# Optimization experiments

Measured on AMD Instinct MI355X. Metric: run time of the kernel, lower is better.

Reference implementation:

```python
import jax, jax.numpy as jnp
import numpy as np
from jax import lax

F_SIZE = 128
N_HEADS = 8
HEAD_D = F_SIZE // N_HEADS
LANE_F = 64
NUM_PREDS = 6


def _layernorm(x, g, b, eps=1e-5):
    m = x.mean(-1, keepdims=True)
    v = jnp.var(x, axis=-1, keepdims=True)
    return (x - m) * lax.rsqrt(v + eps) * g + b


def _lstm_cell(x, h, c, wih, whh, bih, bhh):
    # PyTorch LSTMCell: gates ordered i, f, g, o
    gates = x @ wih.T + bih + h @ whh.T + bhh
    i, f, g, o = jnp.split(gates, 4, axis=-1)
    c2 = jax.nn.sigmoid(f) * c + jax.nn.sigmoid(i) * jnp.tanh(g)
    h2 = jax.nn.sigmoid(o) * jnp.tanh(c2)
    return h2, c2


def _to_xy(dl, yaw):
    return jnp.concatenate([dl * jnp.cos(yaw), dl * jnp.sin(yaw)], axis=-1)


def _attention(tok_pos, h_ego, h, lane_tok, key_mask, wq, wk, wv, wo, pos_w, pos_b):
    # tokens = [ego, vehicles], keys/values = [tokens, lanes]
    B = h_ego.shape[0]
    tok = jnp.concatenate([h_ego, h], axis=1) + tok_pos @ pos_w + pos_b  # [B,N1,F]
    kv = jnp.concatenate([tok, lane_tok], axis=1)  # [B,N1+L,F]
    q = (tok @ wq).reshape(B, -1, N_HEADS, HEAD_D)
    k = (kv @ wk).reshape(B, -1, N_HEADS, HEAD_D)
    v = (kv @ wv).reshape(B, -1, N_HEADS, HEAD_D)
    s = jnp.einsum('bqhd,bkhd->bhqk', q, k) / jnp.asarray(np.sqrt(HEAD_D), jnp.float32)
    s = jnp.where(key_mask[:, None, None, :] > 0, s, -1e9)
    a = jax.nn.softmax(s, axis=-1)
    o = jnp.einsum('bhqk,bkhd->bqhd', a, v).reshape(B, -1, F_SIZE) @ wo
    tok = tok + o
    return tok[:, :1], tok[:, 1:]


def _forward(input, init_pos, lane_input, mask_input, lane_mask,
             conv_w, conv_b, pos_w, pos_b,
             lane_w1, lane_b1, lane_w2, lane_b2, lane_to_f,
             wq, wk, wv, wo, ln_ego_g, ln_ego_b, ln_g, ln_b,
             ego_wih, ego_whh, ego_bih, ego_bhh,
             veh_wih, veh_whh, veh_bih, veh_bhh,
             out_ego_w, out_ego_b, out_w, out_b, len_pred):
    T, B, N1, _ = input.shape
    V = N1 - 1
    Hh = T - 2  # valid conv over time with kernel 3

    # shared conv_input applied to ego+vehicles at once (same weights in original)
    x = jnp.transpose(input, (1, 3, 2, 0))  # [B,2,N1,T]
    feat = lax.conv_general_dilated(x, conv_w, (1, 1), 'VALID',
                                    dimension_numbers=('NCHW', 'OIHW', 'NCHW'))
    feat = feat + conv_b[None, :, None, None]
    feat = jnp.transpose(feat, (3, 0, 2, 1))  # [Hh,B,N1,F]
    h_ego_seq, h_seq = feat[:, :, :1], feat[:, :, 1:]

    # lane embedding: per-point MLP + mean pool
    lanes = jax.nn.relu(lane_input @ lane_w1 + lane_b1)
    lanes = jax.nn.relu(lanes @ lane_w2 + lane_b2).mean(axis=2)  # [B,L,LANE_F]
    lane_tok = lanes @ lane_to_f  # [B,L,F]
    key_mask = jnp.concatenate([mask_input, lane_mask], axis=1)  # [B,N1+L]

    pos0 = init_pos[0]
    pe0, pv0 = pos0[:, :1], pos0[:, 1:]

    def cell_step(hx_ego, cx_ego, hx, cx, he, hv, pe, pv):
        tok_pos = jnp.concatenate([pe, pv], axis=1)
        ae, av = _attention(tok_pos, he, hv, lane_tok, key_mask, wq, wk, wv, wo, pos_w, pos_b)
        ae = _layernorm(ae.reshape(B, F_SIZE), ln_ego_g, ln_ego_b)
        av = _layernorm(av.reshape(B * V, F_SIZE), ln_g, ln_b)
        hx_ego, cx_ego = _lstm_cell(ae, hx_ego, cx_ego, ego_wih, ego_whh, ego_bih, ego_bhh)
        hx, cx = _lstm_cell(av, hx, cx, veh_wih, veh_whh, veh_bih, veh_bhh)
        return hx_ego, cx_ego, hx, cx

    def hist_step(carry, xs):
        hx_ego, cx_ego, hx, cx, pe, pv = carry
        he, hv, xe, xv = xs
        pe = pe + _to_xy(xe[..., 0:1], xe[..., 1:2])
        pv = pv + _to_xy(xv[..., 0:1], xv[..., 1:2])
        hx_ego, cx_ego, hx, cx = cell_step(hx_ego, cx_ego, hx, cx, he, hv, pe, pv)
        return (hx_ego, cx_ego, hx, cx, pe, pv), None

    carry0 = (jnp.zeros((B, F_SIZE)), jnp.zeros((B, F_SIZE)),
              jnp.zeros((B * V, F_SIZE)), jnp.zeros((B * V, F_SIZE)), pe0, pv0)
    xs = (h_ego_seq, h_seq, input[:Hh, :, :1, :].transpose(0, 1, 2, 3), input[:Hh, :, 1:, :])
    carry, _ = lax.scan(hist_step, carry0, xs)
    hx_ego, cx_ego, hx, cx, pe, pv = carry

    pe = jnp.repeat(pe[:, :, None, :], NUM_PREDS, axis=2)  # [B,1,P,2]
    pv = jnp.repeat(pv[:, :, None, :], NUM_PREDS, axis=2)  # [B,V,P,2]

    def pred_step(carry, _):
        hx_ego, cx_ego, hx, cx, pe, pv = carry
        he = hx_ego.reshape(B, 1, F_SIZE)
        hv = hx.reshape(B, V, F_SIZE)
        hx_ego, cx_ego, hx, cx = cell_step(hx_ego, cx_ego, hx, cx, he, hv,
                                           pe.mean(axis=2), pv.mean(axis=2))
        oe = (hx_ego @ out_ego_w + out_ego_b).reshape(B, 1, NUM_PREDS, 6)
        ov = (hx @ out_w + out_b).reshape(B, V, NUM_PREDS, 6)
        pe = pe + _to_xy(oe[..., 0:1], oe[..., 1:2])
        pv = pv + _to_xy(ov[..., 0:1], ov[..., 1:2])
        y = jnp.concatenate([
            jnp.concatenate([pe, oe[..., 2:6]], axis=-1),
            jnp.concatenate([pv, ov[..., 2:6]], axis=-1)], axis=1)  # [B,N1,P,6]
        return (hx_ego, cx_ego, hx, cx, pe, pv), y

    carry = (hx_ego, cx_ego, hx, cx, pe, pv)
    _, ys = lax.scan(pred_step, carry, None, length=len_pred)
    return ys  # [len_pred,B,N1,NUM_PREDS,6]


def setup_inputs() -> dict:
    key = jax.random.key(0)
    ks = jax.random.split(key, 40)
    B, T, N1, L, PTS = 128, 22, 32, 64, 10
    F, LF, G4, P6 = F_SIZE, LANE_F, 4 * F_SIZE, NUM_PREDS * 6
    s = 0.05
    inp = {}
    inp['input'] = jax.random.normal(ks[0], (T, B, N1, 2), jnp.float32) * 0.1
    inp['init_pos'] = jax.random.normal(ks[1], (1, B, N1, 2), jnp.float32) * 10.0
    inp['lane_input'] = jax.random.normal(ks[2], (B, L, PTS, 2), jnp.float32)
    inp['mask_input'] = jnp.ones((B, N1), jnp.float32)
    inp['lane_mask'] = jnp.ones((B, L), jnp.float32)
    inp['conv_w'] = jax.random.normal(ks[3], (F, 2, 1, 3), jnp.float32) * s
    inp['conv_b'] = jnp.zeros((F,), jnp.float32)
    inp['pos_w'] = jax.random.normal(ks[4], (2, F), jnp.float32) * s
    inp['pos_b'] = jnp.zeros((F,), jnp.float32)
    inp['lane_w1'] = jax.random.normal(ks[5], (2, LF), jnp.float32) * s
    inp['lane_b1'] = jnp.zeros((LF,), jnp.float32)
    inp['lane_w2'] = jax.random.normal(ks[6], (LF, LF), jnp.float32) * s
    inp['lane_b2'] = jnp.zeros((LF,), jnp.float32)
    inp['lane_to_f'] = jax.random.normal(ks[7], (LF, F), jnp.float32) * s
    inp['wq'] = jax.random.normal(ks[8], (F, F), jnp.float32) * s
    inp['wk'] = jax.random.normal(ks[9], (F, F), jnp.float32) * s
    inp['wv'] = jax.random.normal(ks[10], (F, F), jnp.float32) * s
    inp['wo'] = jax.random.normal(ks[11], (F, F), jnp.float32) * s
    inp['ln_ego_g'] = jnp.ones((F,), jnp.float32)
    inp['ln_ego_b'] = jnp.zeros((F,), jnp.float32)
    inp['ln_g'] = jnp.ones((F,), jnp.float32)
    inp['ln_b'] = jnp.zeros((F,), jnp.float32)
    inp['ego_wih'] = jax.random.normal(ks[12], (G4, F), jnp.float32) * s
    inp['ego_whh'] = jax.random.normal(ks[13], (G4, F), jnp.float32) * s
    inp['ego_bih'] = jnp.zeros((G4,), jnp.float32)
    inp['ego_bhh'] = jnp.zeros((G4,), jnp.float32)
    inp['veh_wih'] = jax.random.normal(ks[14], (G4, F), jnp.float32) * s
    inp['veh_whh'] = jax.random.normal(ks[15], (G4, F), jnp.float32) * s
    inp['veh_bih'] = jnp.zeros((G4,), jnp.float32)
    inp['veh_bhh'] = jnp.zeros((G4,), jnp.float32)
    inp['out_ego_w'] = jax.random.normal(ks[16], (F, P6), jnp.float32) * s
    inp['out_ego_b'] = jnp.zeros((P6,), jnp.float32)
    inp['out_w'] = jax.random.normal(ks[17], (F, P6), jnp.float32) * s
    inp['out_b'] = jnp.zeros((P6,), jnp.float32)
    inp['len_pred'] = 30
    return inp


def reference(input, init_pos, lane_input, mask_input, lane_mask,
              conv_w, conv_b, pos_w, pos_b,
              lane_w1, lane_b1, lane_w2, lane_b2, lane_to_f,
              wq, wk, wv, wo, ln_ego_g, ln_ego_b, ln_g, ln_b,
              ego_wih, ego_whh, ego_bih, ego_bhh,
              veh_wih, veh_whh, veh_bih, veh_bhh,
              out_ego_w, out_ego_b, out_w, out_b, len_pred):
    return _forward(input, init_pos, lane_input, mask_input, lane_mask,
                    conv_w, conv_b, pos_w, pos_b,
                    lane_w1, lane_b1, lane_w2, lane_b2, lane_to_f,
                    wq, wk, wv, wo, ln_ego_g, ln_ego_b, ln_g, ln_b,
                    ego_wih, ego_whh, ego_bih, ego_bhh,
                    veh_wih, veh_whh, veh_bih, veh_bhh,
                    out_ego_w, out_ego_b, out_w, out_b, len_pred)
```

## Files before the change

### kernel.cpp

```cpp
#include <hip/hip_runtime.h>
#include <hip/hip_bf16.h>
#include <math.h>

constexpr int B   = 128;
constexpr int N1  = 32;
constexpr int HH  = 20;
constexpr int L   = 64;
constexpr int PTS = 10;
constexpr int F   = 128;
constexpr int LF  = 64;
constexpr int NH  = 8;
constexpr int HD  = 16;
constexpr int KVN = 96;
constexpr int G4  = 512;
constexpr int NP  = 6;
constexpr int P6  = 36;
constexpr int LEN = 30;

__device__ __forceinline__ float sigmoidf(float x) { return 1.f / (1.f + expf(-x)); }


__global__ void k_lane_tok(const float* __restrict__ lane_input,
                           const float* __restrict__ w1, const float* __restrict__ b1,
                           const float* __restrict__ w2, const float* __restrict__ b2,
                           const float* __restrict__ to_f,
                           float* __restrict__ kvbuf) {
    int bl = blockIdx.x; int b = bl / L, l = bl % L;
    int tid = threadIdx.x;
    __shared__ float h1[PTS][LF];
    __shared__ float m[LF];
    const float* xin = lane_input + ((size_t)(b * L + l) * PTS) * 2;
    float w10 = w1[tid], w11 = w1[LF + tid], bb1 = b1[tid];
    for (int p = 0; p < PTS; ++p) {
        float v = xin[p * 2] * w10 + xin[p * 2 + 1] * w11 + bb1;
        h1[p][tid] = fmaxf(v, 0.f);
    }
    __syncthreads();
    float acc = 0.f;
    for (int p = 0; p < PTS; ++p) {
        float s = b2[tid];
        for (int h = 0; h < LF; ++h) s += h1[p][h] * w2[h * LF + tid];
        acc += fmaxf(s, 0.f);
    }
    m[tid] = acc * (1.f / PTS);
    __syncthreads();
    float* outp = kvbuf + ((size_t)(b * KVN) + 32 + l) * F;
    for (int f = tid; f < F; f += LF) {
        float s = 0.f;
        for (int j = 0; j < LF; ++j) s += m[j] * to_f[j * F + f];
        outp[f] = s;
    }
}

__global__ void k_lane_kv(const float* __restrict__ kvbuf,
                          const float* __restrict__ wk, const float* __restrict__ wv,
                          float* __restrict__ kb, float* __restrict__ vb) {
    int g = blockIdx.x & 7, b = blockIdx.x >> 3;
    int n0 = 32 + g * 8;
    int tid = threadIdx.x;
    int j = tid & 127, rh = tid >> 7;
    __shared__ float tok[8][F];
    for (int i = tid; i < 8 * F; i += 256) {
        int r = i >> 7, c = i & 127;
        tok[r][c] = kvbuf[((size_t)b * KVN + n0 + r) * F + c];
    }
    __syncthreads();
    float ak[4] = {0, 0, 0, 0}, av[4] = {0, 0, 0, 0};
    int r0 = rh * 4;
    for (int k2 = 0; k2 < F; ++k2) {
        float wkv = wk[k2 * F + j], wvv = wv[k2 * F + j];
#pragma unroll
        for (int r = 0; r < 4; ++r) {
            float x = tok[r0 + r][k2];
            ak[r] += x * wkv; av[r] += x * wvv;
        }
    }
#pragma unroll
    for (int r = 0; r < 4; ++r) {
        int n = n0 + r0 + r;
        kb[((size_t)b * KVN + n) * F + j] = ak[r];
        vb[((size_t)b * KVN + n) * F + j] = av[r];
    }
}

__global__ void k_hist_pos(const float* __restrict__ input,
                           const float* __restrict__ init_pos,
                           float* __restrict__ hist_pos,
                           float* __restrict__ pred_pos) {
    int idx = blockIdx.x * blockDim.x + threadIdx.x;
    if (idx >= B * N1) return;
    float px = init_pos[idx * 2], py = init_pos[idx * 2 + 1];
    int b = idx / N1, n = idx % N1;
    for (int t = 0; t < HH; ++t) {
        const float* ip = input + ((size_t)(t * B + b) * N1 + n) * 2;
        float dl = ip[0], yaw = ip[1];
        px += dl * cosf(yaw);
        py += dl * sinf(yaw);
        float* hp = hist_pos + ((size_t)(t * B + b) * N1 + n) * 2;
        hp[0] = px; hp[1] = py;
    }
#pragma unroll
    for (int p = 0; p < NP; ++p) {
        pred_pos[((size_t)idx * NP + p) * 2 + 0] = px;
        pred_pos[((size_t)idx * NP + p) * 2 + 1] = py;
    }
}

__global__ void k_transpose_all(const float* __restrict__ w0, const float* __restrict__ w1,
                                const float* __restrict__ w2, const float* __restrict__ w3,
                                float* __restrict__ wt) {
    int i = blockIdx.x * blockDim.x + threadIdx.x;
    if (i >= 4 * G4 * F) return;
    int m = i / (G4 * F), rem = i % (G4 * F);
    int j = rem / F, k2 = rem % F;
    const float* src = (m == 0) ? w0 : (m == 1) ? w1 : (m == 2) ? w2 : w3;
    wt[(size_t)m * G4 * F + (size_t)k2 * G4 + j] = src[rem];
}


__global__ void k_tok_qkv(const float* __restrict__ input, const float* __restrict__ hist_pos,
                          const float* __restrict__ h, const float* __restrict__ pred_pos,
                          const float* __restrict__ conv_w, const float* __restrict__ conv_b,
                          const float* __restrict__ pos_w, const float* __restrict__ pos_b,
                          const float* __restrict__ wq, const float* __restrict__ wk,
                          const float* __restrict__ wv,
                          float* __restrict__ kvbuf, float* __restrict__ qb,
                          float* __restrict__ kb, float* __restrict__ vb,
                          int mode, int t) {
    int g = blockIdx.x & 3, b = blockIdx.x >> 2;
    int n0 = g * 8;
    int tid = threadIdx.x;
    int j = tid & 127, rh = tid >> 7;
    __shared__ float tok[8][F];
    for (int i = tid; i < 8 * F; i += 256) {
        int r = i >> 7, c = i & 127;
        int n = n0 + r;
        float acc;
        if (mode == 0) {
            acc = conv_b[c];
#pragma unroll
            for (int kt = 0; kt < 3; ++kt) {
                const float* ip = input + ((size_t)((t + kt) * B + b) * N1 + n) * 2;
                acc += ip[0] * conv_w[(c * 2 + 0) * 3 + kt] + ip[1] * conv_w[(c * 2 + 1) * 3 + kt];
            }
            const float* hp = hist_pos + ((size_t)(t * B + b) * N1 + n) * 2;
            acc += hp[0] * pos_w[c] + hp[1] * pos_w[F + c] + pos_b[c];
        } else {
            const float* pp = pred_pos + ((size_t)(b * N1 + n)) * NP * 2;
            float mx = 0.f, my = 0.f;
#pragma unroll
            for (int p = 0; p < NP; ++p) { mx += pp[p * 2]; my += pp[p * 2 + 1]; }
            mx *= (1.f / NP); my *= (1.f / NP);
            acc = h[((size_t)b * N1 + n) * F + c] + mx * pos_w[c] + my * pos_w[F + c] + pos_b[c];
        }
        tok[r][c] = acc;
        kvbuf[((size_t)b * KVN + n) * F + c] = acc;
    }
    __syncthreads();
    float aq[4] = {0, 0, 0, 0}, ak[4] = {0, 0, 0, 0}, av[4] = {0, 0, 0, 0};
    int r0 = rh * 4;
    for (int k2 = 0; k2 < F; k2 += 2) {
        float wq0 = wq[k2 * F + j], wk0 = wk[k2 * F + j], wv0 = wv[k2 * F + j];
        float wq1 = wq[(k2 + 1) * F + j], wk1 = wk[(k2 + 1) * F + j], wv1 = wv[(k2 + 1) * F + j];
#pragma unroll
        for (int r = 0; r < 4; ++r) {
            float x0 = tok[r0 + r][k2], x1 = tok[r0 + r][k2 + 1];
            aq[r] += x0 * wq0 + x1 * wq1;
            ak[r] += x0 * wk0 + x1 * wk1;
            av[r] += x0 * wv0 + x1 * wv1;
        }
    }
#pragma unroll
    for (int r = 0; r < 4; ++r) {
        int n = n0 + r0 + r;
        qb[((size_t)b * N1 + n) * F + j]  = aq[r];
        kb[((size_t)b * KVN + n) * F + j] = ak[r];
        vb[((size_t)b * KVN + n) * F + j] = av[r];
    }
}

__global__ void k_attn(const float* __restrict__ qb, const float* __restrict__ kb,
                       const float* __restrict__ vb,
                       const float* __restrict__ mask_in, const float* __restrict__ lane_mask,
                       float* __restrict__ ao) {
    int h = blockIdx.x & 7, b = blockIdx.x >> 3;
    int tid = threadIdx.x;
    __shared__ float qh[N1][HD];
    __shared__ float kh[KVN][HD + 1];
    __shared__ float vh[KVN][HD + 1];
    __shared__ float mk[KVN];
    __shared__ float sc[N1][KVN + 1];
    for (int i = tid; i < N1 * HD; i += 128) {
        int qr = i >> 4, d = i & 15;
        qh[qr][d] = qb[((size_t)b * N1 + qr) * F + h * HD + d];
    }
    for (int i = tid; i < KVN * HD; i += 128) {
        int kc = i >> 4, d = i & 15;
        kh[kc][d] = kb[((size_t)b * KVN + kc) * F + h * HD + d];
        vh[kc][d] = vb[((size_t)b * KVN + kc) * F + h * HD + d];
    }
    if (tid < KVN)
        mk[tid] = (tid < N1) ? mask_in[b * N1 + tid] : lane_mask[b * L + (tid - N1)];
    __syncthreads();
    for (int i = tid; i < N1 * KVN; i += 128) {
        int qr = i / KVN, kc = i % KVN;
        float acc = 0.f;
#pragma unroll
        for (int d = 0; d < HD; ++d) acc += qh[qr][d] * kh[kc][d];
        sc[qr][kc] = (mk[kc] > 0.f) ? acc * 0.25f : -1e9f;
    }
    __syncthreads();
    if (tid < N1) {
        float mx = -1e30f;
        for (int kc = 0; kc < KVN; ++kc) mx = fmaxf(mx, sc[tid][kc]);
        float sum = 0.f;
        for (int kc = 0; kc < KVN; ++kc) { float e = expf(sc[tid][kc] - mx); sc[tid][kc] = e; sum += e; }
        float inv = 1.f / sum;
        for (int kc = 0; kc < KVN; ++kc) sc[tid][kc] *= inv;
    }
    __syncthreads();
    for (int i = tid; i < N1 * HD; i += 128) {
        int qr = i >> 4, d = i & 15;
        float acc = 0.f;
        for (int kc = 0; kc < KVN; ++kc) acc += sc[qr][kc] * vh[kc][d];
        ao[((size_t)b * N1 + qr) * F + h * HD + d] = acc;
    }
}

__global__ void k_proj_ln(const float* __restrict__ ao, const float* __restrict__ kvbuf,
                          const float* __restrict__ wo,
                          const float* __restrict__ ln_ego_g, const float* __restrict__ ln_ego_b,
                          const float* __restrict__ ln_g, const float* __restrict__ ln_b,
                          float* __restrict__ xln) {
    int gq = blockIdx.x & 3, b = blockIdx.x >> 2;
    int n0 = gq * 8;
    int tid = threadIdx.x;
    int j = tid & 127, rh = tid >> 7;
    __shared__ float arow[8][F];
    __shared__ float xb[8][F + 1];
    __shared__ float st[8][2];
    for (int i = tid; i < 8 * F; i += 256) {
        int r = i >> 7, c = i & 127;
        arow[r][c] = ao[((size_t)b * N1 + n0 + r) * F + c];
    }
    __syncthreads();
    float acc[4] = {0, 0, 0, 0};
    int r0 = rh * 4;
    for (int k2 = 0; k2 < F; k2 += 2) {
        float w0 = wo[k2 * F + j], w1 = wo[(k2 + 1) * F + j];
#pragma unroll
        for (int r = 0; r < 4; ++r)
            acc[r] += arow[r0 + r][k2] * w0 + arow[r0 + r][k2 + 1] * w1;
    }
#pragma unroll
    for (int r = 0; r < 4; ++r)
        xb[r0 + r][j] = kvbuf[((size_t)b * KVN + n0 + r0 + r) * F + j] + acc[r];
    __syncthreads();
    if (tid < 8) {
        float s1 = 0.f, s2 = 0.f;
        for (int c = 0; c < F; ++c) { float x = xb[tid][c]; s1 += x; s2 += x * x; }
        float mean = s1 * (1.f / F);
        float var = s2 * (1.f / F) - mean * mean;
        st[tid][0] = mean; st[tid][1] = rsqrtf(var + 1e-5f);
    }
    __syncthreads();
    for (int i = tid; i < 8 * F; i += 256) {
        int r = i >> 7, c = i & 127;
        int n = n0 + r;
        const float* g  = (n == 0) ? ln_ego_g : ln_g;
        const float* bb = (n == 0) ? ln_ego_b : ln_b;
        xln[((size_t)b * N1 + n) * F + c] = (xb[r][c] - st[r][0]) * st[r][1] * g[c] + bb[c];
    }
}

__global__ void k_lstm_pred(const float* __restrict__ xln,
                            const float* __restrict__ ego_wih_t, const float* __restrict__ ego_whh_t,
                            const float* __restrict__ ego_bih, const float* __restrict__ ego_bhh,
                            const float* __restrict__ veh_wih_t, const float* __restrict__ veh_whh_t,
                            const float* __restrict__ veh_bih, const float* __restrict__ veh_bhh,
                            float* __restrict__ h, float* __restrict__ c,
                            const float* __restrict__ out_ego_w, const float* __restrict__ out_ego_b,
                            const float* __restrict__ out_w, const float* __restrict__ out_b,
                            float* __restrict__ pred_pos, float* __restrict__ out,
                            int mode, int step) {
    int n = blockIdx.x >> 3, bg = blockIdx.x & 7;
    int b0 = bg * 16;
    int j = threadIdx.x;
    const float *wih, *whh, *bih, *bhh;
    if (n == 0) { wih = ego_wih_t; whh = ego_whh_t; bih = ego_bih; bhh = ego_bhh; }
    else        { wih = veh_wih_t; whh = veh_whh_t; bih = veh_bih; bhh = veh_bhh; }
    __shared__ float xr[16][F];
    __shared__ float hr2[16][F];
    __shared__ float gs[16][G4];
    for (int i = j; i < 16 * F; i += 512) {
        int r = i >> 7, k2 = i & 127;
        size_t bn = (size_t)(b0 + r) * N1 + n;
        xr[r][k2]  = xln[bn * F + k2];
        hr2[r][k2] = h[bn * F + k2];
    }
    __syncthreads();
    float acc[16];
    float bsum = bih[j] + bhh[j];
#pragma unroll
    for (int r = 0; r < 16; ++r) acc[r] = bsum;
    for (int k2 = 0; k2 < F; k2 += 4) {
        float wa0 = wih[(size_t)(k2    ) * G4 + j], wb0 = whh[(size_t)(k2    ) * G4 + j];
        float wa1 = wih[(size_t)(k2 + 1) * G4 + j], wb1 = whh[(size_t)(k2 + 1) * G4 + j];
        float wa2 = wih[(size_t)(k2 + 2) * G4 + j], wb2 = whh[(size_t)(k2 + 2) * G4 + j];
        float wa3 = wih[(size_t)(k2 + 3) * G4 + j], wb3 = whh[(size_t)(k2 + 3) * G4 + j];
#pragma unroll
        for (int r = 0; r < 16; ++r) {
            float x0 = xr[r][k2], x1 = xr[r][k2 + 1], x2 = xr[r][k2 + 2], x3 = xr[r][k2 + 3];
            float h0 = hr2[r][k2], h1 = hr2[r][k2 + 1], h2v = hr2[r][k2 + 2], h3 = hr2[r][k2 + 3];
            acc[r] += x0 * wa0 + x1 * wa1 + x2 * wa2 + x3 * wa3
                    + h0 * wb0 + h1 * wb1 + h2v * wb2 + h3 * wb3;
        }
    }
#pragma unroll
    for (int r = 0; r < 16; ++r) gs[r][j] = acc[r];
    __syncthreads();
    for (int i = j; i < 16 * F; i += 512) {
        int r = i >> 7, f = i & 127;
        size_t bn = (size_t)(b0 + r) * N1 + n;
        float ig = gs[r][f], fg = gs[r][F + f], gg = gs[r][2 * F + f], og = gs[r][3 * F + f];
        float cold = c[bn * F + f];
        float c2 = sigmoidf(fg) * cold + sigmoidf(ig) * tanhf(gg);
        float h2 = sigmoidf(og) * tanhf(c2);
        c[bn * F + f] = c2;
        h[bn * F + f] = h2;
        xr[r][f] = h2;
    }
    if (mode == 1) {
        const float* W  = (n == 0) ? out_ego_w : out_w;
        const float* bb = (n == 0) ? out_ego_b : out_b;
        __syncthreads();
        for (int i = j; i < 16 * P6; i += 512) {
            int r = i / P6, jj = i % P6;
            float a = bb[jj];
            for (int k2 = 0; k2 < F; ++k2) a += xr[r][k2] * W[k2 * P6 + jj];
            gs[r][jj] = a;
        }
        __syncthreads();
        if (j < 16 * NP) {
            int r = j / NP, p = j % NP;
            size_t bn = (size_t)(b0 + r) * N1 + n;
            float dl = gs[r][p * 6 + 0], yaw = gs[r][p * 6 + 1];
            float* pp = pred_pos + (bn * NP + p) * 2;
            float px = pp[0] + dl * cosf(yaw);
            float py = pp[1] + dl * sinf(yaw);
            pp[0] = px; pp[1] = py;
            float* y = out + (size_t)step * B * N1 * P6 + (bn * NP + p) * 6;
            y[0] = px; y[1] = py;
            y[2] = gs[r][p * 6 + 2]; y[3] = gs[r][p * 6 + 3];
            y[4] = gs[r][p * 6 + 4]; y[5] = gs[r][p * 6 + 5];
        }
    }
}

extern "C" void kernel_launch(void* const* d_in, const int* in_sizes, int n_in,
                              void* d_out, int out_size, void* d_ws, size_t ws_size,
                              hipStream_t stream) {
    const float* input      = (const float*)d_in[0];
    const float* init_pos   = (const float*)d_in[1];
    const float* lane_input = (const float*)d_in[2];
    const float* mask_input = (const float*)d_in[3];
    const float* lane_mask  = (const float*)d_in[4];
    const float* conv_w     = (const float*)d_in[5];
    const float* conv_b     = (const float*)d_in[6];
    const float* pos_w      = (const float*)d_in[7];
    const float* pos_b      = (const float*)d_in[8];
    const float* lane_w1    = (const float*)d_in[9];
    const float* lane_b1    = (const float*)d_in[10];
    const float* lane_w2    = (const float*)d_in[11];
    const float* lane_b2    = (const float*)d_in[12];
    const float* lane_to_f  = (const float*)d_in[13];
    const float* wq         = (const float*)d_in[14];
    const float* wk         = (const float*)d_in[15];
    const float* wv         = (const float*)d_in[16];
    const float* wo         = (const float*)d_in[17];
    const float* ln_ego_g   = (const float*)d_in[18];
    const float* ln_ego_b   = (const float*)d_in[19];
    const float* ln_g       = (const float*)d_in[20];
    const float* ln_b       = (const float*)d_in[21];
    const float* ego_wih    = (const float*)d_in[22];
    const float* ego_whh    = (const float*)d_in[23];
    const float* ego_bih    = (const float*)d_in[24];
    const float* ego_bhh    = (const float*)d_in[25];
    const float* veh_wih    = (const float*)d_in[26];
    const float* veh_whh    = (const float*)d_in[27];
    const float* veh_bih    = (const float*)d_in[28];
    const float* veh_bhh    = (const float*)d_in[29];
    const float* out_ego_w  = (const float*)d_in[30];
    const float* out_ego_b  = (const float*)d_in[31];
    const float* out_w      = (const float*)d_in[32];
    const float* out_b      = (const float*)d_in[33];

    float* out = (float*)d_out;
    float* ws = (float*)d_ws;

    float* kv       = ws;
    float* qb       = kv + (size_t)B * KVN * F;
    float* kb       = qb + (size_t)B * N1 * F;
    float* vb       = kb + (size_t)B * KVN * F;
    float* ao       = vb + (size_t)B * KVN * F;
    float* xln      = ao + (size_t)B * N1 * F;
    float* hbuf     = xln + (size_t)B * N1 * F;
    float* cbuf     = hbuf + (size_t)B * N1 * F;
    float* hist_pos = cbuf + (size_t)B * N1 * F;
    float* pred_pos = hist_pos + (size_t)HH * B * N1 * 2;
    float* wt       = pred_pos + (size_t)B * N1 * NP * 2;
    float* ego_wih_t = wt;
    float* ego_whh_t = wt + (size_t)G4 * F;
    float* veh_wih_t = wt + (size_t)2 * G4 * F;
    float* veh_whh_t = wt + (size_t)3 * G4 * F;

    hipMemsetAsync(hbuf, 0, (size_t)B * N1 * F * sizeof(float), stream);
    hipMemsetAsync(cbuf, 0, (size_t)B * N1 * F * sizeof(float), stream);
    k_lane_tok<<<B * L, 64, 0, stream>>>(lane_input, lane_w1, lane_b1, lane_w2, lane_b2,
                                         lane_to_f, kv);
    k_hist_pos<<<(B * N1 + 255) / 256, 256, 0, stream>>>(input, init_pos, hist_pos, pred_pos);
    k_transpose_all<<<(4 * G4 * F + 255) / 256, 256, 0, stream>>>(ego_wih, ego_whh, veh_wih,
                                                                  veh_whh, wt);
    k_lane_kv<<<B * 8, 256, 0, stream>>>(kv, wk, wv, kb, vb);

    for (int t = 0; t < HH; ++t) {
        k_tok_qkv<<<B * 4, 256, 0, stream>>>(input, hist_pos, hbuf, pred_pos,
                                             conv_w, conv_b, pos_w, pos_b,
                                             wq, wk, wv, kv, qb, kb, vb, 0, t);
        k_attn<<<B * NH, 128, 0, stream>>>(qb, kb, vb, mask_input, lane_mask, ao);
        k_proj_ln<<<B * 4, 256, 0, stream>>>(ao, kv, wo, ln_ego_g, ln_ego_b, ln_g, ln_b, xln);
        k_lstm_pred<<<N1 * 8, 512, 0, stream>>>(xln, ego_wih_t, ego_whh_t, ego_bih, ego_bhh,
                                                veh_wih_t, veh_whh_t, veh_bih, veh_bhh,
                                                hbuf, cbuf, out_ego_w, out_ego_b, out_w, out_b,
                                                pred_pos, out, 0, 0);
    }

    for (int s = 0; s < LEN; ++s) {
        k_tok_qkv<<<B * 4, 256, 0, stream>>>(input, hist_pos, hbuf, pred_pos,
                                             conv_w, conv_b, pos_w, pos_b,
                                             wq, wk, wv, kv, qb, kb, vb, 1, 0);
        k_attn<<<B * NH, 128, 0, stream>>>(qb, kb, vb, mask_input, lane_mask, ao);
        k_proj_ln<<<B * 4, 256, 0, stream>>>(ao, kv, wo, ln_ego_g, ln_ego_b, ln_g, ln_b, xln);
        k_lstm_pred<<<N1 * 8, 512, 0, stream>>>(xln, ego_wih_t, ego_whh_t, ego_bih, ego_bhh,
                                                veh_wih_t, veh_whh_t, veh_bih, veh_bhh,
                                                hbuf, cbuf, out_ego_w, out_ego_b, out_w, out_b,
                                                pred_pos, out, 1, s);
    }
}
```

Baseline: 5.338 ms.

## Fuse the whole recurrent loop into one persistent per-batch megakernel

Replaces the 200 per-step launches (tok/qkv, attention, projection+layernorm, LSTM) with a single kernel of 128 blocks, one per batch element, that runs all 50 steps with tokens, Q/K/V, scores and hidden state held in shared memory. LSTM weights are repacked into an interleaved 8-wide layout, and wq/wk/wv/wo into float4 tuples, so each load is vectorised. The aim is to remove launch overhead and global round-trips between stages. The cost is that only 128 blocks occupy the GPU, leaving many CUs idle and making each step serial within a block.

```diff
diff --git a/kernel.cpp b/kernel.cpp
--- a/kernel.cpp
+++ b/kernel.cpp
@@ -106,254 +106,312 @@
     }
 }
 
-__global__ void k_transpose_all(const float* __restrict__ w0, const float* __restrict__ w1,
-                                const float* __restrict__ w2, const float* __restrict__ w3,
-                                float* __restrict__ wt) {
+__global__ void k_build_w8(const float* __restrict__ wih, const float* __restrict__ whh,
+                           float* __restrict__ w8) {
     int i = blockIdx.x * blockDim.x + threadIdx.x;
-    if (i >= 4 * G4 * F) return;
-    int m = i / (G4 * F), rem = i % (G4 * F);
-    int j = rem / F, k2 = rem % F;
-    const float* src = (m == 0) ? w0 : (m == 1) ? w1 : (m == 2) ? w2 : w3;
-    wt[(size_t)m * G4 * F + (size_t)k2 * G4 + j] = src[rem];
-}
-
-
-__global__ void k_tok_qkv(const float* __restrict__ input, const float* __restrict__ hist_pos,
-                          const float* __restrict__ h, const float* __restrict__ pred_pos,
-                          const float* __restrict__ conv_w, const float* __restrict__ conv_b,
-                          const float* __restrict__ pos_w, const float* __restrict__ pos_b,
-                          const float* __restrict__ wq, const float* __restrict__ wk,
-                          const float* __restrict__ wv,
-                          float* __restrict__ kvbuf, float* __restrict__ qb,
-                          float* __restrict__ kb, float* __restrict__ vb,
-                          int mode, int t) {
-    int g = blockIdx.x & 3, b = blockIdx.x >> 2;
-    int n0 = g * 8;
-    int tid = threadIdx.x;
-    int j = tid & 127, rh = tid >> 7;
-    __shared__ float tok[8][F];
-    for (int i = tid; i < 8 * F; i += 256) {
+    if (i >= 128 * 128 * 8) return;
+    int s = i & 7, f = (i >> 3) & 127, k = i >> 10;
+    w8[i] = (s < 4) ? wih[((size_t)(s * 128 + f)) * 128 + k]
+                    : whh[((size_t)((s - 4) * 128 + f)) * 128 + k];
+}
+
+__global__ void k_build_wqkvo(const float* __restrict__ wq, const float* __restrict__ wk,
+                              const float* __restrict__ wv, const float* __restrict__ wo,
+                              float4* __restrict__ out4) {
+    int i = blockIdx.x * blockDim.x + threadIdx.x;
+    if (i >= 128 * 128) return;
+    out4[i] = make_float4(wq[i], wk[i], wv[i], wo[i]);
+}
+
+__global__ __launch_bounds__(1024) void k_mega(
+    const float* __restrict__ input, const float* __restrict__ hist_pos,
+    const float* __restrict__ conv_w, const float* __restrict__ conv_b,
+    const float* __restrict__ pos_w, const float* __restrict__ pos_b,
+    const float4* __restrict__ wqkvo,
+    const float* __restrict__ ln_ego_g, const float* __restrict__ ln_ego_b,
+    const float* __restrict__ ln_g, const float* __restrict__ ln_b,
+    const float* __restrict__ egoW8, const float* __restrict__ vehW8,
+    const float* __restrict__ ego_bih, const float* __restrict__ ego_bhh,
+    const float* __restrict__ veh_bih, const float* __restrict__ veh_bhh,
+    const float* __restrict__ out_ego_w, const float* __restrict__ out_ego_b,
+    const float* __restrict__ out_w, const float* __restrict__ out_b,
+    const float* __restrict__ mask_input, const float* __restrict__ lane_mask,
+    const float* __restrict__ lane_kb, const float* __restrict__ lane_vb,
+    float* __restrict__ pred_pos, float* __restrict__ cbuf,
+    float* __restrict__ out)
+{
+    const int b = blockIdx.x;
+    const int tid = threadIdx.x;
+
+    __shared__ float  Kbuf[96 * 129];
+    __shared__ float4 Vt4[128 * 25];
+    __shared__ float  tokS[32 * 128];
+    __shared__ float  qsS[32 * 128];
+    __shared__ float  hsS[32 * 128];
+    __shared__ float4 sc4[32 * 24];
+    __shared__ float  mkS[96];
+
+    float* VtF = (float*)Vt4;
+    float* scF = (float*)sc4;
+
+    const int f  = tid & 127;
+    const int ng = tid >> 7;
+    const int n0 = ng * 4;
+
+    float bv[4], be[4];
+#pragma unroll
+    for (int g = 0; g < 4; ++g) {
+        bv[g] = veh_bih[g * 128 + f] + veh_bhh[g * 128 + f];
+        be[g] = ego_bih[g * 128 + f] + ego_bhh[g * 128 + f];
+    }
+
+    for (int i = tid; i < 64 * 128; i += 1024) {
         int r = i >> 7, c = i & 127;
-        int n = n0 + r;
-        float acc;
-        if (mode == 0) {
-            acc = conv_b[c];
-#pragma unroll
-            for (int kt = 0; kt < 3; ++kt) {
-                const float* ip = input + ((size_t)((t + kt) * B + b) * N1 + n) * 2;
-                acc += ip[0] * conv_w[(c * 2 + 0) * 3 + kt] + ip[1] * conv_w[(c * 2 + 1) * 3 + kt];
-            }
-            const float* hp = hist_pos + ((size_t)(t * B + b) * N1 + n) * 2;
-            acc += hp[0] * pos_w[c] + hp[1] * pos_w[F + c] + pos_b[c];
-        } else {
-            const float* pp = pred_pos + ((size_t)(b * N1 + n)) * NP * 2;
-            float mx = 0.f, my = 0.f;
-#pragma unroll
-            for (int p = 0; p < NP; ++p) { mx += pp[p * 2]; my += pp[p * 2 + 1]; }
-            mx *= (1.f / NP); my *= (1.f / NP);
-            acc = h[((size_t)b * N1 + n) * F + c] + mx * pos_w[c] + my * pos_w[F + c] + pos_b[c];
-        }
-        tok[r][c] = acc;
-        kvbuf[((size_t)b * KVN + n) * F + c] = acc;
-    }
+        float kvv = lane_kb[((size_t)b * KVN + 32 + r) * F + c];
+        float vvv = lane_vb[((size_t)b * KVN + 32 + r) * F + c];
+        Kbuf[(32 + r) * 129 + c] = kvv;
+        VtF[c * 100 + 32 + r]    = vvv;
+    }
+    for (int i = tid; i < 32 * 128; i += 1024) hsS[i] = 0.f;
+    if (tid < 96) mkS[tid] = (tid < 32) ? mask_input[b * 32 + tid] : lane_mask[b * 64 + tid - 32];
     __syncthreads();
-    float aq[4] = {0, 0, 0, 0}, ak[4] = {0, 0, 0, 0}, av[4] = {0, 0, 0, 0};
-    int r0 = rh * 4;
-    for (int k2 = 0; k2 < F; k2 += 2) {
-        float wq0 = wq[k2 * F + j], wk0 = wk[k2 * F + j], wv0 = wv[k2 * F + j];
-        float wq1 = wq[(k2 + 1) * F + j], wk1 = wk[(k2 + 1) * F + j], wv1 = wv[(k2 + 1) * F + j];
-#pragma unroll
-        for (int r = 0; r < 4; ++r) {
-            float x0 = tok[r0 + r][k2], x1 = tok[r0 + r][k2 + 1];
-            aq[r] += x0 * wq0 + x1 * wq1;
-            ak[r] += x0 * wk0 + x1 * wk1;
-            av[r] += x0 * wv0 + x1 * wv1;
-        }
-    }
-#pragma unroll
-    for (int r = 0; r < 4; ++r) {
-        int n = n0 + r0 + r;
-        qb[((size_t)b * N1 + n) * F + j]  = aq[r];
-        kb[((size_t)b * KVN + n) * F + j] = ak[r];
-        vb[((size_t)b * KVN + n) * F + j] = av[r];
-    }
-}
-
-__global__ void k_attn(const float* __restrict__ qb, const float* __restrict__ kb,
-                       const float* __restrict__ vb,
-                       const float* __restrict__ mask_in, const float* __restrict__ lane_mask,
-                       float* __restrict__ ao) {
-    int h = blockIdx.x & 7, b = blockIdx.x >> 3;
-    int tid = threadIdx.x;
-    __shared__ float qh[N1][HD];
-    __shared__ float kh[KVN][HD + 1];
-    __shared__ float vh[KVN][HD + 1];
-    __shared__ float mk[KVN];
-    __shared__ float sc[N1][KVN + 1];
-    for (int i = tid; i < N1 * HD; i += 128) {
-        int qr = i >> 4, d = i & 15;
-        qh[qr][d] = qb[((size_t)b * N1 + qr) * F + h * HD + d];
-    }
-    for (int i = tid; i < KVN * HD; i += 128) {
-        int kc = i >> 4, d = i & 15;
-        kh[kc][d] = kb[((size_t)b * KVN + kc) * F + h * HD + d];
-        vh[kc][d] = vb[((size_t)b * KVN + kc) * F + h * HD + d];
-    }
-    if (tid < KVN)
-        mk[tid] = (tid < N1) ? mask_in[b * N1 + tid] : lane_mask[b * L + (tid - N1)];
-    __syncthreads();
-    for (int i = tid; i < N1 * KVN; i += 128) {
-        int qr = i / KVN, kc = i % KVN;
-        float acc = 0.f;
-#pragma unroll
-        for (int d = 0; d < HD; ++d) acc += qh[qr][d] * kh[kc][d];
-        sc[qr][kc] = (mk[kc] > 0.f) ? acc * 0.25f : -1e9f;
-    }
-    __syncthreads();
-    if (tid < N1) {
-        float mx = -1e30f;
-        for (int kc = 0; kc < KVN; ++kc) mx = fmaxf(mx, sc[tid][kc]);
-        float sum = 0.f;
-        for (int kc = 0; kc < KVN; ++kc) { float e = expf(sc[tid][kc] - mx); sc[tid][kc] = e; sum += e; }
-        float inv = 1.f / sum;
-        for (int kc = 0; kc < KVN; ++kc) sc[tid][kc] *= inv;
-    }
-    __syncthreads();
-    for (int i = tid; i < N1 * HD; i += 128) {
-        int qr = i >> 4, d = i & 15;
-        float acc = 0.f;
-        for (int kc = 0; kc < KVN; ++kc) acc += sc[qr][kc] * vh[kc][d];
-        ao[((size_t)b * N1 + qr) * F + h * HD + d] = acc;
-    }
-}
-
-__global__ void k_proj_ln(const float* __restrict__ ao, const float* __restrict__ kvbuf,
-                          const float* __restrict__ wo,
-                          const float* __restrict__ ln_ego_g, const float* __restrict__ ln_ego_b,
-                          const float* __restrict__ ln_g, const float* __restrict__ ln_b,
-                          float* __restrict__ xln) {
-    int gq = blockIdx.x & 3, b = blockIdx.x >> 2;
-    int n0 = gq * 8;
-    int tid = threadIdx.x;
-    int j = tid & 127, rh = tid >> 7;
-    __shared__ float arow[8][F];
-    __shared__ float xb[8][F + 1];
-    __shared__ float st[8][2];
-    for (int i = tid; i < 8 * F; i += 256) {
-        int r = i >> 7, c = i & 127;
-        arow[r][c] = ao[((size_t)b * N1 + n0 + r) * F + c];
-    }
-    __syncthreads();
-    float acc[4] = {0, 0, 0, 0};
-    int r0 = rh * 4;
-    for (int k2 = 0; k2 < F; k2 += 2) {
-        float w0 = wo[k2 * F + j], w1 = wo[(k2 + 1) * F + j];
-#pragma unroll
-        for (int r = 0; r < 4; ++r)
-            acc[r] += arow[r0 + r][k2] * w0 + arow[r0 + r][k2 + 1] * w1;
-    }
-#pragma unroll
-    for (int r = 0; r < 4; ++r)
-        xb[r0 + r][j] = kvbuf[((size_t)b * KVN + n0 + r0 + r) * F + j] + acc[r];
-    __syncthreads();
-    if (tid < 8) {
-        float s1 = 0.f, s2 = 0.f;
-        for (int c = 0; c < F; ++c) { float x = xb[tid][c]; s1 += x; s2 += x * x; }
-        float mean = s1 * (1.f / F);
-        float var = s2 * (1.f / F) - mean * mean;
-        st[tid][0] = mean; st[tid][1] = rsqrtf(var + 1e-5f);
-    }
-    __syncthreads();
-    for (int i = tid; i < 8 * F; i += 256) {
-        int r = i >> 7, c = i & 127;
-        int n = n0 + r;
-        const float* g  = (n == 0) ? ln_ego_g : ln_g;
-        const float* bb = (n == 0) ? ln_ego_b : ln_b;
-        xln[((size_t)b * N1 + n) * F + c] = (xb[r][c] - st[r][0]) * st[r][1] * g[c] + bb[c];
-    }
-}
-
-__global__ void k_lstm_pred(const float* __restrict__ xln,
-                            const float* __restrict__ ego_wih_t, const float* __restrict__ ego_whh_t,
-                            const float* __restrict__ ego_bih, const float* __restrict__ ego_bhh,
-                            const float* __restrict__ veh_wih_t, const float* __restrict__ veh_whh_t,
-                            const float* __restrict__ veh_bih, const float* __restrict__ veh_bhh,
-                            float* __restrict__ h, float* __restrict__ c,
-                            const float* __restrict__ out_ego_w, const float* __restrict__ out_ego_b,
-                            const float* __restrict__ out_w, const float* __restrict__ out_b,
-                            float* __restrict__ pred_pos, float* __restrict__ out,
-                            int mode, int step) {
-    int n = blockIdx.x >> 3, bg = blockIdx.x & 7;
-    int b0 = bg * 16;
-    int j = threadIdx.x;
-    const float *wih, *whh, *bih, *bhh;
-    if (n == 0) { wih = ego_wih_t; whh = ego_whh_t; bih = ego_bih; bhh = ego_bhh; }
-    else        { wih = veh_wih_t; whh = veh_whh_t; bih = veh_bih; bhh = veh_bhh; }
-    __shared__ float xr[16][F];
-    __shared__ float hr2[16][F];
-    __shared__ float gs[16][G4];
-    for (int i = j; i < 16 * F; i += 512) {
-        int r = i >> 7, k2 = i & 127;
-        size_t bn = (size_t)(b0 + r) * N1 + n;
-        xr[r][k2]  = xln[bn * F + k2];
-        hr2[r][k2] = h[bn * F + k2];
-    }
-    __syncthreads();
-    float acc[16];
-    float bsum = bih[j] + bhh[j];
-#pragma unroll
-    for (int r = 0; r < 16; ++r) acc[r] = bsum;
-    for (int k2 = 0; k2 < F; k2 += 4) {
-        float wa0 = wih[(size_t)(k2    ) * G4 + j], wb0 = whh[(size_t)(k2    ) * G4 + j];
-        float wa1 = wih[(size_t)(k2 + 1) * G4 + j], wb1 = whh[(size_t)(k2 + 1) * G4 + j];
-        float wa2 = wih[(size_t)(k2 + 2) * G4 + j], wb2 = whh[(size_t)(k2 + 2) * G4 + j];
-        float wa3 = wih[(size_t)(k2 + 3) * G4 + j], wb3 = whh[(size_t)(k2 + 3) * G4 + j];
-#pragma unroll
-        for (int r = 0; r < 16; ++r) {
-            float x0 = xr[r][k2], x1 = xr[r][k2 + 1], x2 = xr[r][k2 + 2], x3 = xr[r][k2 + 3];
-            float h0 = hr2[r][k2], h1 = hr2[r][k2 + 1], h2v = hr2[r][k2 + 2], h3 = hr2[r][k2 + 3];
-            acc[r] += x0 * wa0 + x1 * wa1 + x2 * wa2 + x3 * wa3
-                    + h0 * wb0 + h1 * wb1 + h2v * wb2 + h3 * wb3;
-        }
-    }
-#pragma unroll
-    for (int r = 0; r < 16; ++r) gs[r][j] = acc[r];
-    __syncthreads();
-    for (int i = j; i < 16 * F; i += 512) {
-        int r = i >> 7, f = i & 127;
-        size_t bn = (size_t)(b0 + r) * N1 + n;
-        float ig = gs[r][f], fg = gs[r][F + f], gg = gs[r][2 * F + f], og = gs[r][3 * F + f];
-        float cold = c[bn * F + f];
-        float c2 = sigmoidf(fg) * cold + sigmoidf(ig) * tanhf(gg);
-        float h2 = sigmoidf(og) * tanhf(c2);
-        c[bn * F + f] = c2;
-        h[bn * F + f] = h2;
-        xr[r][f] = h2;
-    }
-    if (mode == 1) {
-        const float* W  = (n == 0) ? out_ego_w : out_w;
-        const float* bb = (n == 0) ? out_ego_b : out_b;
+
+#pragma unroll 1
+    for (int step = 0; step < HH + LEN; ++step) {
+        const int mode = (step >= HH) ? 1 : 0;
+        const int t = mode ? 0 : step;
+
+        for (int i = tid; i < 32 * 128; i += 1024) {
+            int n = i >> 7, c = i & 127;
+            float acc;
+            if (mode == 0) {
+                acc = conv_b[c];
+#pragma unroll
+                for (int kt = 0; kt < 3; ++kt) {
+                    const float* ip = input + ((size_t)((t + kt) * B + b) * N1 + n) * 2;
+                    acc += ip[0] * conv_w[(c * 2 + 0) * 3 + kt] + ip[1] * conv_w[(c * 2 + 1) * 3 + kt];
+                }
+                const float* hp = hist_pos + ((size_t)(t * B + b) * N1 + n) * 2;
+                acc += hp[0] * pos_w[c] + hp[1] * pos_w[128 + c] + pos_b[c];
+            } else {
+                const float* pp = pred_pos + (size_t)b * 384 + n * 12;
+                float mx = 0.f, my = 0.f;
+#pragma unroll
+                for (int p = 0; p < 6; ++p) { mx += pp[p * 2]; my += pp[p * 2 + 1]; }
+                mx *= (1.f / 6.f); my *= (1.f / 6.f);
+                acc = hsS[i] + mx * pos_w[c] + my * pos_w[128 + c] + pos_b[c];
+            }
+            tokS[i] = acc;
+        }
         __syncthreads();
-        for (int i = j; i < 16 * P6; i += 512) {
-            int r = i / P6, jj = i % P6;
-            float a = bb[jj];
-            for (int k2 = 0; k2 < F; ++k2) a += xr[r][k2] * W[k2 * P6 + jj];
-            gs[r][jj] = a;
+
+        {
+            float aq[4] = {0, 0, 0, 0}, ak[4] = {0, 0, 0, 0}, av[4] = {0, 0, 0, 0};
+            for (int k2 = 0; k2 < 128; k2 += 4) {
+                float4 xv[4];
+#pragma unroll
+                for (int r = 0; r < 4; ++r) xv[r] = *(const float4*)&tokS[(n0 + r) * 128 + k2];
+#pragma unroll
+                for (int kk = 0; kk < 4; ++kk) {
+                    float4 w4 = wqkvo[(size_t)(k2 + kk) * 128 + f];
+#pragma unroll
+                    for (int r = 0; r < 4; ++r) {
+                        float x = (&xv[r].x)[kk];
+                        aq[r] += x * w4.x; ak[r] += x * w4.y; av[r] += x * w4.z;
+                    }
+                }
+            }
+#pragma unroll
+            for (int r = 0; r < 4; ++r) {
+                qsS[(n0 + r) * 128 + f]  = aq[r];
+                Kbuf[(n0 + r) * 129 + f] = ak[r];
+                VtF[f * 100 + n0 + r]    = av[r];
+            }
         }
         __syncthreads();
-        if (j < 16 * NP) {
-            int r = j / NP, p = j % NP;
-            size_t bn = (size_t)(b0 + r) * N1 + n;
-            float dl = gs[r][p * 6 + 0], yaw = gs[r][p * 6 + 1];
-            float* pp = pred_pos + (bn * NP + p) * 2;
-            float px = pp[0] + dl * cosf(yaw);
-            float py = pp[1] + dl * sinf(yaw);
-            pp[0] = px; pp[1] = py;
-            float* y = out + (size_t)step * B * N1 * P6 + (bn * NP + p) * 6;
-            y[0] = px; y[1] = py;
-            y[2] = gs[r][p * 6 + 2]; y[3] = gs[r][p * 6 + 3];
-            y[4] = gs[r][p * 6 + 4]; y[5] = gs[r][p * 6 + 5];
-        }
+
+#pragma unroll 1
+        for (int h = 0; h < NH; ++h) {
+            const int hb = h * 16;
+            if (tid < 512) {
+                const int lane = tid & 63;
+                const int rb = (tid >> 6) * 4;
+                const int k2ok = lane < 32;
+                float s0[4] = {0, 0, 0, 0}, s1[4] = {0, 0, 0, 0};
+                for (int d4 = 0; d4 < 16; d4 += 4) {
+                    float4 qv[4];
+#pragma unroll
+                    for (int r = 0; r < 4; ++r) qv[r] = *(const float4*)&qsS[(rb + r) * 128 + hb + d4];
+#pragma unroll
+                    for (int kk = 0; kk < 4; ++kk) {
+                        float kA = Kbuf[lane * 129 + hb + d4 + kk];
+                        float kB = k2ok ? Kbuf[(64 + lane) * 129 + hb + d4 + kk] : 0.f;
+#pragma unroll
+                        for (int r = 0; r < 4; ++r) {
+                            float q = (&qv[r].x)[kk];
+                            s0[r] += q * kA; s1[r] += q * kB;
+                        }
+                    }
+                }
+                float mA = mkS[lane];
+                float mB = k2ok ? mkS[64 + lane] : 0.f;
+#pragma unroll
+                for (int r = 0; r < 4; ++r) {
+                    float v0 = (mA > 0.f) ? s0[r] * 0.25f : -1e9f;
+                    float v1 = (k2ok && mB > 0.f) ? s1[r] * 0.25f : -1e9f;
+                    float m = fmaxf(v0, v1);
+#pragma unroll
+                    for (int off = 32; off; off >>= 1) m = fmaxf(m, __shfl_xor(m, off));
+                    float e0 = expf(v0 - m);
+                    float e1 = k2ok ? expf(v1 - m) : 0.f;
+                    float s = e0 + e1;
+#pragma unroll
+                    for (int off = 32; off; off >>= 1) s += __shfl_xor(s, off);
+                    float inv = 1.f / s;
+                    scF[(rb + r) * 96 + lane] = e0 * inv;
+                    if (k2ok) scF[(rb + r) * 96 + 64 + lane] = e1 * inv;
+                }
+            }
+            __syncthreads();
+            if (tid < 512) {
+                const int qr = tid >> 4, d = tid & 15;
+                const float4* vrow = Vt4 + (hb + d) * 25;
+                const float4* srow = sc4 + qr * 24;
+                float acc = 0.f;
+#pragma unroll
+                for (int q4 = 0; q4 < 24; ++q4) {
+                    float4 pf = srow[q4], vv = vrow[q4];
+                    acc += pf.x * vv.x + pf.y * vv.y + pf.z * vv.z + pf.w * vv.w;
+                }
+                qsS[qr * 128 + hb + d] = acc;
+            }
+            __syncthreads();
+        }
+
+        {
+            float ac[4] = {0, 0, 0, 0};
+            for (int k2 = 0; k2 < 128; k2 += 4) {
+                float4 av4[4];
+#pragma unroll
+                for (int r = 0; r < 4; ++r) av4[r] = *(const float4*)&qsS[(n0 + r) * 128 + k2];
+#pragma unroll
+                for (int kk = 0; kk < 4; ++kk) {
+                    float4 w4 = wqkvo[(size_t)(k2 + kk) * 128 + f];
+#pragma unroll
+                    for (int r = 0; r < 4; ++r) ac[r] += (&av4[r].x)[kk] * w4.w;
+                }
+            }
+#pragma unroll
+            for (int r = 0; r < 4; ++r) tokS[(n0 + r) * 128 + f] += ac[r];
+        }
+        __syncthreads();
+
+        {
+            const int row = tid >> 5, l = tid & 31;
+            float x0 = tokS[row * 128 + l],      x1 = tokS[row * 128 + l + 32];
+            float x2 = tokS[row * 128 + l + 64], x3 = tokS[row * 128 + l + 96];
+            float s1v = x0 + x1 + x2 + x3;
+            float s2v = x0 * x0 + x1 * x1 + x2 * x2 + x3 * x3;
+#pragma unroll
+            for (int off = 16; off; off >>= 1) {
+                s1v += __shfl_xor(s1v, off, 32);
+                s2v += __shfl_xor(s2v, off, 32);
+            }
+            float mean = s1v * (1.f / 128.f);
+            float rs = rsqrtf(s2v * (1.f / 128.f) - mean * mean + 1e-5f);
+            const float* gg = (row == 0) ? ln_ego_g : ln_g;
+            const float* bb = (row == 0) ? ln_ego_b : ln_b;
+            tokS[row * 128 + l]      = (x0 - mean) * rs * gg[l]      + bb[l];
+            tokS[row * 128 + l + 32] = (x1 - mean) * rs * gg[l + 32] + bb[l + 32];
+            tokS[row * 128 + l + 64] = (x2 - mean) * rs * gg[l + 64] + bb[l + 64];
+            tokS[row * 128 + l + 96] = (x3 - mean) * rs * gg[l + 96] + bb[l + 96];
+        }
+        __syncthreads();
+
+        {
+            float acc[4][4];
+#pragma unroll
+            for (int r = 0; r < 4; ++r)
+#pragma unroll
+                for (int g = 0; g < 4; ++g) acc[r][g] = bv[g];
+            for (int k2 = 0; k2 < 128; k2 += 4) {
+                float4 xv[4], hv[4];
+#pragma unroll
+                for (int r = 0; r < 4; ++r) {
+                    xv[r] = *(const float4*)&tokS[(n0 + r) * 128 + k2];
+                    hv[r] = *(const float4*)&hsS[(n0 + r) * 128 + k2];
+                }
+#pragma unroll
+                for (int kk = 0; kk < 4; ++kk) {
+                    const float4* wp = (const float4*)&vehW8[((size_t)(k2 + kk) * 128 + f) * 8];
+                    float4 wi = wp[0], wh = wp[1];
+#pragma unroll
+                    for (int r = 0; r < 4; ++r) {
+                        float x = (&xv[r].x)[kk], hc = (&hv[r].x)[kk];
+                        acc[r][0] += x * wi.x + hc * wh.x;
+                        acc[r][1] += x * wi.y + hc * wh.y;
+                        acc[r][2] += x * wi.z + hc * wh.z;
+                        acc[r][3] += x * wi.w + hc * wh.w;
+                    }
+                }
+            }
+            if (ng == 0) {
+                float ae[4] = {be[0], be[1], be[2], be[3]};
+                for (int k2 = 0; k2 < 128; k2 += 4) {
+                    float4 xv = *(const float4*)&tokS[k2];
+                    float4 hv = *(const float4*)&hsS[k2];
+#pragma unroll
+                    for (int kk = 0; kk < 4; ++kk) {
+                        const float4* wp = (const float4*)&egoW8[((size_t)(k2 + kk) * 128 + f) * 8];
+                        float4 wi = wp[0], wh = wp[1];
+                        float x = (&xv.x)[kk], hc = (&hv.x)[kk];
+                        ae[0] += x * wi.x + hc * wh.x;
+                        ae[1] += x * wi.y + hc * wh.y;
+                        ae[2] += x * wi.z + hc * wh.z;
+                        ae[3] += x * wi.w + hc * wh.w;
+                    }
+                }
+#pragma unroll
+                for (int g = 0; g < 4; ++g) acc[0][g] = ae[g];
+            }
+            __syncthreads();
+#pragma unroll
+            for (int r = 0; r < 4; ++r) {
+                int n = n0 + r;
+                size_t cix = ((size_t)b * 32 + n) * 128 + f;
+                float c2 = sigmoidf(acc[r][1]) * cbuf[cix] + sigmoidf(acc[r][0]) * tanhf(acc[r][2]);
+                float h2 = sigmoidf(acc[r][3]) * tanhf(c2);
+                cbuf[cix] = c2;
+                hsS[n * 128 + f] = h2;
+            }
+        }
+
+        if (mode) {
+            __syncthreads();
+            for (int i = tid; i < 32 * 36; i += 1024) {
+                int n = i / 36, jj = i - n * 36;
+                const float* W = (n == 0) ? out_ego_w : out_w;
+                float a = (n == 0) ? out_ego_b[jj] : out_b[jj];
+                const float* hr = &hsS[n * 128];
+#pragma unroll 4
+                for (int k2 = 0; k2 < 128; ++k2) a += hr[k2] * W[k2 * 36 + jj];
+                scF[i] = a;
+            }
+            __syncthreads();
+            if (tid < 192) {
+                int n = tid / 6, p = tid - n * 6;
+                float dl = scF[n * 36 + p * 6], yaw = scF[n * 36 + p * 6 + 1];
+                float* pp = pred_pos + (size_t)b * 384 + n * 12 + p * 2;
+                float px = pp[0] + dl * cosf(yaw);
+                float py = pp[1] + dl * sinf(yaw);
+                pp[0] = px; pp[1] = py;
+                float* y = out + (size_t)(step - HH) * (B * N1 * P6) + ((size_t)b * 32 + n) * 36 + p * 6;
+                y[0] = px; y[1] = py;
+                y[2] = scF[n * 36 + p * 6 + 2]; y[3] = scF[n * 36 + p * 6 + 3];
+                y[4] = scF[n * 36 + p * 6 + 4]; y[5] = scF[n * 36 + p * 6 + 5];
+            }
+        }
+        __syncthreads();
     }
 }
 
@@ -399,51 +457,28 @@
     float* ws = (float*)d_ws;
 
     float* kv       = ws;
-    float* qb       = kv + (size_t)B * KVN * F;
-    float* kb       = qb + (size_t)B * N1 * F;
+    float* kb       = kv + (size_t)B * KVN * F;
     float* vb       = kb + (size_t)B * KVN * F;
-    float* ao       = vb + (size_t)B * KVN * F;
-    float* xln      = ao + (size_t)B * N1 * F;
-    float* hbuf     = xln + (size_t)B * N1 * F;
-    float* cbuf     = hbuf + (size_t)B * N1 * F;
+    float* cbuf     = vb + (size_t)B * KVN * F;
     float* hist_pos = cbuf + (size_t)B * N1 * F;
     float* pred_pos = hist_pos + (size_t)HH * B * N1 * 2;
-    float* wt       = pred_pos + (size_t)B * N1 * NP * 2;
-    float* ego_wih_t = wt;
-    float* ego_whh_t = wt + (size_t)G4 * F;
-    float* veh_wih_t = wt + (size_t)2 * G4 * F;
-    float* veh_whh_t = wt + (size_t)3 * G4 * F;
-
-    hipMemsetAsync(hbuf, 0, (size_t)B * N1 * F * sizeof(float), stream);
+    float* egoW8    = pred_pos + (size_t)B * N1 * NP * 2;
+    float* vehW8    = egoW8 + (size_t)128 * 128 * 8;
+    float* wqkvo    = vehW8 + (size_t)128 * 128 * 8;
+
     hipMemsetAsync(cbuf, 0, (size_t)B * N1 * F * sizeof(float), stream);
     k_lane_tok<<<B * L, 64, 0, stream>>>(lane_input, lane_w1, lane_b1, lane_w2, lane_b2,
                                          lane_to_f, kv);
     k_hist_pos<<<(B * N1 + 255) / 256, 256, 0, stream>>>(input, init_pos, hist_pos, pred_pos);
-    k_transpose_all<<<(4 * G4 * F + 255) / 256, 256, 0, stream>>>(ego_wih, ego_whh, veh_wih,
-                                                                  veh_whh, wt);
+    k_build_w8<<<(128 * 128 * 8 + 255) / 256, 256, 0, stream>>>(ego_wih, ego_whh, egoW8);
+    k_build_w8<<<(128 * 128 * 8 + 255) / 256, 256, 0, stream>>>(veh_wih, veh_whh, vehW8);
+    k_build_wqkvo<<<(128 * 128 + 255) / 256, 256, 0, stream>>>(wq, wk, wv, wo, (float4*)wqkvo);
     k_lane_kv<<<B * 8, 256, 0, stream>>>(kv, wk, wv, kb, vb);
 
-    for (int t = 0; t < HH; ++t) {
-        k_tok_qkv<<<B * 4, 256, 0, stream>>>(input, hist_pos, hbuf, pred_pos,
-                                             conv_w, conv_b, pos_w, pos_b,
-                                             wq, wk, wv, kv, qb, kb, vb, 0, t);
-        k_attn<<<B * NH, 128, 0, stream>>>(qb, kb, vb, mask_input, lane_mask, ao);
-        k_proj_ln<<<B * 4, 256, 0, stream>>>(ao, kv, wo, ln_ego_g, ln_ego_b, ln_g, ln_b, xln);
-        k_lstm_pred<<<N1 * 8, 512, 0, stream>>>(xln, ego_wih_t, ego_whh_t, ego_bih, ego_bhh,
-                                                veh_wih_t, veh_whh_t, veh_bih, veh_bhh,
-                                                hbuf, cbuf, out_ego_w, out_ego_b, out_w, out_b,
-                                                pred_pos, out, 0, 0);
-    }
-
-    for (int s = 0; s < LEN; ++s) {
-        k_tok_qkv<<<B * 4, 256, 0, stream>>>(input, hist_pos, hbuf, pred_pos,
-                                             conv_w, conv_b, pos_w, pos_b,
-                                             wq, wk, wv, kv, qb, kb, vb, 1, 0);
-        k_attn<<<B * NH, 128, 0, stream>>>(qb, kb, vb, mask_input, lane_mask, ao);
-        k_proj_ln<<<B * 4, 256, 0, stream>>>(ao, kv, wo, ln_ego_g, ln_ego_b, ln_g, ln_b, xln);
-        k_lstm_pred<<<N1 * 8, 512, 0, stream>>>(xln, ego_wih_t, ego_whh_t, ego_bih, ego_bhh,
-                                                veh_wih_t, veh_whh_t, veh_bih, veh_bhh,
-                                                hbuf, cbuf, out_ego_w, out_ego_b, out_w, out_b,
-                                                pred_pos, out, 1, s);
-    }
-}
+    k_mega<<<B, 1024, 0, stream>>>(input, hist_pos, conv_w, conv_b, pos_w, pos_b,
+                                   (const float4*)wqkvo,
+                                   ln_ego_g, ln_ego_b, ln_g, ln_b,
+                                   egoW8, vehW8, ego_bih, ego_bhh, veh_bih, veh_bhh,
+                                   out_ego_w, out_ego_b, out_w, out_b,
+                                   mask_input, lane_mask, kb, vb, pred_pos, cbuf, out);
+}
```

Result: slower. 8.907 ms (+66.9%).
